# Performance work log

Hardware: AMD Instinct MI355X
Metric: run time of the kernel (lower is better)

The kernel has to match this reference:

```python
import jax, jax.numpy as jnp
import numpy as np

B, N, E = 128, 256, 2048
BINS = 16

def _gcn(x, src, dst, W, b):
    # GCNConv with self-loops and symmetric deg^-1/2 normalization (PyG default).
    h = x @ W  # [N, Fout]
    deg = jnp.zeros(x.shape[0], x.dtype).at[dst].add(1.0) + 1.0  # +1 self-loop
    dinv = jax.lax.rsqrt(deg)
    coef = dinv[src] * dinv[dst]  # [E]
    agg = jnp.zeros_like(h).at[dst].add(h[src] * coef[:, None])
    return agg + h / deg[:, None] + b  # self-loop norm = 1/deg

def _gnn(x, ei, W1, b1, W2, b2, W3, b3):
    # x: [B,N,Fin], ei: [B,2,E]. Dropout skipped (eval mode).
    def single(x, ei):
        s, d = ei[0], ei[1]
        h = jax.nn.relu(_gcn(x, s, d, W1, b1))
        h = jax.nn.relu(_gcn(h, s, d, W2, b2))
        return _gcn(h, s, d, W3, b3)
    return jax.vmap(single)(x, ei)

def _att_pool(x, Watt):
    # SimGNN attention pooling; all graphs have exactly N nodes.
    ctx = jnp.tanh((x @ Watt.T).sum(axis=1) / jnp.asarray(N, x.dtype))  # [B,f3]
    scores = jax.nn.sigmoid(jnp.einsum('bnf,bf->bn', x, ctx))  # [B,N]
    return jnp.einsum('bnf,bn->bf', x, scores)  # [B,f3]

def _forward(xq, xc, eq, ec, W1, b1, W2, b2, W3, b3, Watt, ntnW, ntnV, ntnb, fc1W, fc1b, fc2W, fc2b):
    q = _gnn(xq, eq, W1, b1, W2, b2, W3, b3)  # [B,N,f3]
    c = _gnn(xc, ec, W1, b1, W2, b2, W3, b3)
    e1 = _att_pool(q, Watt)
    e2 = _att_pool(c, Watt)
    # NTN: bilinear + linear on concat + bias
    scores = jax.nn.relu(
        jnp.einsum('bi,tij,bj->bt', e1, ntnW, e2)
        + jnp.concatenate([e1, e2], axis=-1) @ ntnV.T
        + ntnb
    )  # [B, tensor_neurons]
    # histogram of all pairwise node-embedding dot products (torch.histc semantics)
    s = jnp.einsum('bnf,bmf->bnm', q, c).ravel()
    lo, hi = s.min(), s.max()
    idx = jnp.clip(jnp.floor((s - lo) / (hi - lo) * BINS).astype(jnp.int32), 0, BINS - 1)
    counts = jnp.zeros(BINS, s.dtype).at[idx].add(1.0)
    h = jax.lax.stop_gradient(counts / counts.sum())
    scores = jnp.concatenate([scores, jnp.broadcast_to(h, (scores.shape[0], BINS))], axis=1)
    scores = jax.nn.relu(scores @ fc1W.T + fc1b)
    p = jax.nn.sigmoid(scores @ fc2W.T + fc2b)  # [B,1]
    return p.squeeze()


def setup_inputs() -> dict:
    key = jax.random.key(0)
    ks = jax.random.split(key, 20)
    Fin, f1, f2, f3, T, BN = 128, 128, 64, 32, 16, 16
    def xav(k, shape):
        fan_in, fan_out = shape[-1], shape[0]
        lim = np.sqrt(6.0 / (fan_in + fan_out))
        return jax.random.uniform(k, shape, jnp.float32, -lim, lim)
    return {
        'xq': jax.random.normal(ks[0], (B, N, Fin), jnp.float32),
        'xc': jax.random.normal(ks[1], (B, N, Fin), jnp.float32),
        'eq': jax.random.randint(ks[2], (B, 2, E), 0, N, jnp.int32),
        'ec': jax.random.randint(ks[3], (B, 2, E), 0, N, jnp.int32),
        'W1': xav(ks[4], (Fin, f1)), 'b1': jnp.zeros((f1,), jnp.float32),
        'W2': xav(ks[5], (f1, f2)), 'b2': jnp.zeros((f2,), jnp.float32),
        'W3': xav(ks[6], (f2, f3)), 'b3': jnp.zeros((f3,), jnp.float32),
        'Watt': xav(ks[7], (f3, f3)),
        'ntnW': xav(ks[8], (T, f3, f3)),
        'ntnV': xav(ks[9], (T, 2 * f3)),
        'ntnb': xav(ks[10], (T, 1)).squeeze(-1),
        'fc1W': xav(ks[11], (BN, T + BINS)), 'fc1b': jnp.zeros((BN,), jnp.float32),
        'fc2W': xav(ks[12], (1, BN)), 'fc2b': jnp.zeros((1,), jnp.float32),
    }


def reference(xq, xc, eq, ec, W1, b1, W2, b2, W3, b3, Watt, ntnW, ntnV, ntnb, fc1W, fc1b, fc2W, fc2b):
    return _forward(xq, xc, eq, ec, W1, b1, W2, b2, W3, b3, Watt, ntnW, ntnV, ntnb, fc1W, fc1b, fc2W, fc2b)
```

## Files before the change

### kernel.cpp

```cpp
#include <hip/hip_runtime.h>
#include <math.h>

#define BB 128
#define NN 256
#define EE 2048
#define BINS 16

__global__ void csr_kernel(const int* __restrict__ eq, const int* __restrict__ ec,
                           int* __restrict__ off, int* __restrict__ srcs,
                           float* __restrict__ wts) {
    int g = blockIdx.x;
    int b = g < BB ? g : g - BB;
    const int* ei = g < BB ? eq : ec;
    int t = threadIdx.x;
    __shared__ int cnt[NN];
    __shared__ int sa[NN], sb[NN];
    __shared__ int cursor[NN];
    __shared__ float dvs[NN];
    cnt[t] = 0;
    __syncthreads();
    const int* src = ei + b * 2 * EE;
    const int* dst = src + EE;
    for (int e = t; e < EE; e += 256) atomicAdd(&cnt[dst[e]], 1);
    __syncthreads();
    dvs[t] = rsqrtf((float)cnt[t] + 1.0f);
    sa[t] = cnt[t];
    __syncthreads();
    int* pin = sa; int* pout = sb;
    for (int d = 1; d < NN; d <<= 1) {
        int v = pin[t];
        if (t >= d) v += pin[t - d];
        pout[t] = v;
        __syncthreads();
        int* tmp = pin; pin = pout; pout = tmp;
    }
    int excl = pin[t] - cnt[t];
    off[g * 257 + t] = excl;
    if (t == 255) off[g * 257 + 256] = EE;
    cursor[t] = excl;
    __syncthreads();
    for (int e = t; e < EE; e += 256) {
        int d = dst[e], s = src[e];
        int pos = atomicAdd(&cursor[d], 1);
        srcs[g * EE + pos] = s;
        wts[g * EE + pos] = dvs[s] * dvs[d];
    }
}

template<int FIN, int FOUT, bool RELU>
__global__ __launch_bounds__(512) void gcn_fused(
        const float* __restrict__ X0, const float* __restrict__ X1,
        const float* __restrict__ W, const float* __restrict__ bias,
        const int* __restrict__ off, const int* __restrict__ srcs,
        const float* __restrict__ wts, float* __restrict__ OUT) {
    int blk = blockIdx.x;
    int g = blk % (2 * BB);
    int cb = (blk / (2 * BB)) * 32;
    int t = threadIdx.x;

    __shared__ float hT[NN * 33];
    __shared__ float xsT[16 * 260];
    __shared__ float wt[16 * 32];
    __shared__ int   eoff[NN + 1];
    __shared__ int   esrc[EE];
    __shared__ float ewt[EE];

    const float* xg = (g < BB) ? (X0 + (size_t)g * NN * FIN)
                               : (X1 + (size_t)(g - BB) * NN * FIN);
    const int* o = off + g * 257;
    const int* sr = srcs + (size_t)g * EE;
    const float* wg = wts + (size_t)g * EE;

    for (int i = t; i < EE; i += 512) { esrc[i] = sr[i]; ewt[i] = wg[i]; }
    for (int i = t; i <= NN; i += 512) eoff[i] = o[i];

    int l = t & 63;
    int wv = t >> 6;

    float acc[4][4];
#pragma unroll
    for (int i = 0; i < 4; i++)
#pragma unroll
        for (int j = 0; j < 4; j++) acc[i][j] = 0.f;

    int sn = t >> 1, qk = (t & 1) * 8;
    const float* xr = xg + sn * FIN + qk;
    float4 v0 = *(const float4*)xr;
    float4 v1 = *(const float4*)(xr + 4);
    float wreg = W[(t >> 5) * FOUT + cb + (t & 31)];

    for (int k0 = 0; k0 < FIN; k0 += 16) {
        xsT[(qk + 0) * 260 + sn] = v0.x;
        xsT[(qk + 1) * 260 + sn] = v0.y;
        xsT[(qk + 2) * 260 + sn] = v0.z;
        xsT[(qk + 3) * 260 + sn] = v0.w;
        xsT[(qk + 4) * 260 + sn] = v1.x;
        xsT[(qk + 5) * 260 + sn] = v1.y;
        xsT[(qk + 6) * 260 + sn] = v1.z;
        xsT[(qk + 7) * 260 + sn] = v1.w;
        wt[t] = wreg;
        __syncthreads();
        if (k0 + 16 < FIN) {
            xr += 16;
            v0 = *(const float4*)xr;
            v1 = *(const float4*)(xr + 4);
            wreg = W[(k0 + 16 + (t >> 5)) * FOUT + cb + (t & 31)];
        }
#pragma unroll
        for (int k = 0; k < 16; k++) {
            float4 xv = *(const float4*)&xsT[k * 260 + 4 * l];
            float4 wvv = *(const float4*)&wt[k * 32 + 4 * wv];
            acc[0][0] += xv.x * wvv.x; acc[0][1] += xv.x * wvv.y;
            acc[0][2] += xv.x * wvv.z; acc[0][3] += xv.x * wvv.w;
            acc[1][0] += xv.y * wvv.x; acc[1][1] += xv.y * wvv.y;
            acc[1][2] += xv.y * wvv.z; acc[1][3] += xv.y * wvv.w;
            acc[2][0] += xv.z * wvv.x; acc[2][1] += xv.z * wvv.y;
            acc[2][2] += xv.z * wvv.z; acc[2][3] += xv.z * wvv.w;
            acc[3][0] += xv.w * wvv.x; acc[3][1] += xv.w * wvv.y;
            acc[3][2] += xv.w * wvv.z; acc[3][3] += xv.w * wvv.w;
        }
        __syncthreads();
    }
#pragma unroll
    for (int i = 0; i < 4; i++)
#pragma unroll
        for (int j = 0; j < 4; j++)
            hT[(4 * l + i) * 33 + 4 * wv + j] = acc[i][j];
    __syncthreads();

    int c = t & 31, ng = t >> 5;
    float bb_ = bias[cb + c];
    float* outp = OUT + (size_t)g * NN * FOUT;
    for (int n = ng; n < NN; n += 16) {
        int j0 = eoff[n], j1 = eoff[n + 1];
        float a = 0.f;
        for (int j = j0; j < j1; j++) a += hT[esrc[j] * 33 + c] * ewt[j];
        float d0 = rsqrtf((float)(j1 - j0) + 1.0f);
        float val = a + hT[n * 33 + c] * d0 * d0 + bb_;
        if (RELU) val = fmaxf(val, 0.f);
        outp[n * FOUT + cb + c] = val;
    }
}

__global__ void attpool_kernel(const float* __restrict__ X, const float* __restrict__ Watt,
                               float* __restrict__ e) {
    int g = blockIdx.x;
    int t = threadIdx.x;
    __shared__ float xs[NN * 33];
    __shared__ float red[256];
    __shared__ float mean_s[32], ctx_s[32], sc[NN];
    const float* x = X + (size_t)g * NN * 32;
    for (int i = t; i < NN * 32; i += 256) { int n = i >> 5, c = i & 31; xs[n * 33 + c] = x[i]; }
    __syncthreads();
    {
        int c = t & 31, p = t >> 5;
        float s = 0.f;
        for (int n = p * 32; n < (p + 1) * 32; n++) s += xs[n * 33 + c];
        red[t] = s;
    }
    __syncthreads();
    if (t < 32) {
        float m = 0.f;
        for (int p = 0; p < 8; p++) m += red[p * 32 + t];
        mean_s[t] = m / (float)NN;
    }
    __syncthreads();
    if (t < 32) {
        float a = 0.f;
        for (int f = 0; f < 32; f++) a += mean_s[f] * Watt[t * 32 + f];
        ctx_s[t] = tanhf(a);
    }
    __syncthreads();
    {
        float a = 0.f;
        for (int f = 0; f < 32; f++) a += xs[t * 33 + f] * ctx_s[f];
        sc[t] = 1.f / (1.f + expf(-a));
    }
    __syncthreads();
    {
        int c = t & 31, p = t >> 5;
        float s = 0.f;
        for (int n = p * 32; n < (p + 1) * 32; n++) s += xs[n * 33 + c] * sc[n];
        red[t] = s;
    }
    __syncthreads();
    if (t < 32) {
        float s = 0.f;
        for (int p = 0; p < 8; p++) s += red[p * 32 + t];
        e[g * 32 + t] = s;
    }
}

__global__ void pairdot_minmax(const float* __restrict__ Q, const float* __restrict__ C,
                               float* __restrict__ bmin, float* __restrict__ bmax) {
    int blk = blockIdx.x;
    int b = blk / 16;
    int tn = (blk % 16) >> 2, tm = blk & 3;
    __shared__ float qs[64 * 33], cs[64 * 33];
    int t = threadIdx.x;
    const float* q = Q + ((size_t)b * NN + tn * 64) * 32;
    const float* c = C + ((size_t)b * NN + tm * 64) * 32;
    for (int i = t; i < 64 * 32; i += 256) {
        int n = i >> 5, f = i & 31;
        qs[n * 33 + f] = q[i];
        cs[n * 33 + f] = c[i];
    }
    __syncthreads();
    int m = t & 63, n0 = t >> 6;
    float acc[16];
#pragma unroll
    for (int i = 0; i < 16; i++) acc[i] = 0.f;
    for (int f = 0; f < 32; f++) {
        float cv = cs[m * 33 + f];
#pragma unroll
        for (int i = 0; i < 16; i++) acc[i] += qs[(n0 + 4 * i) * 33 + f] * cv;
    }
    float lmin = acc[0], lmax = acc[0];
#pragma unroll
    for (int i = 1; i < 16; i++) {
        lmin = fminf(lmin, acc[i]);
        lmax = fmaxf(lmax, acc[i]);
    }
    __shared__ float rmin[256], rmax[256];
    rmin[t] = lmin; rmax[t] = lmax;
    __syncthreads();
    for (int s = 128; s > 0; s >>= 1) {
        if (t < s) { rmin[t] = fminf(rmin[t], rmin[t + s]); rmax[t] = fmaxf(rmax[t], rmax[t + s]); }
        __syncthreads();
    }
    if (t == 0) { bmin[blk] = rmin[0]; bmax[blk] = rmax[0]; }
}

__global__ void minmax_kernel(const float* __restrict__ bmin, const float* __restrict__ bmax,
                              float* __restrict__ lohi, float* __restrict__ counts) {
    __shared__ float rmin[256], rmax[256];
    int t = threadIdx.x;
    float lmin = 1e30f, lmax = -1e30f;
    for (int i = t; i < 2048; i += 256) { lmin = fminf(lmin, bmin[i]); lmax = fmaxf(lmax, bmax[i]); }
    rmin[t] = lmin; rmax[t] = lmax;
    __syncthreads();
    for (int s = 128; s > 0; s >>= 1) {
        if (t < s) { rmin[t] = fminf(rmin[t], rmin[t + s]); rmax[t] = fmaxf(rmax[t], rmax[t + s]); }
        __syncthreads();
    }
    if (t == 0) { lohi[0] = rmin[0]; lohi[1] = rmax[0]; }
    if (t < BINS) counts[t] = 0.f;
}

__global__ void pairdot_hist(const float* __restrict__ Q, const float* __restrict__ C,
                             const float* __restrict__ lohi, float* __restrict__ counts) {
    int blk = blockIdx.x;
    int b = blk / 16;
    int tn = (blk % 16) >> 2, tm = blk & 3;
    __shared__ float qs[64 * 33], cs[64 * 33];
    int t = threadIdx.x;
    const float* q = Q + ((size_t)b * NN + tn * 64) * 32;
    const float* c = C + ((size_t)b * NN + tm * 64) * 32;
    for (int i = t; i < 64 * 32; i += 256) {
        int n = i >> 5, f = i & 31;
        qs[n * 33 + f] = q[i];
        cs[n * 33 + f] = c[i];
    }
    __syncthreads();
    int m = t & 63, n0 = t >> 6;
    float acc[16];
#pragma unroll
    for (int i = 0; i < 16; i++) acc[i] = 0.f;
    for (int f = 0; f < 32; f++) {
        float cv = cs[m * 33 + f];
#pragma unroll
        for (int i = 0; i < 16; i++) acc[i] += qs[(n0 + 4 * i) * 33 + f] * cv;
    }
    float lo = lohi[0], hi = lohi[1];
    float scale = (float)BINS / (hi - lo);
    int lane = t & 63;
    int cnt = 0;
#pragma unroll
    for (int i = 0; i < 16; i++) {
        int idx = (int)floorf((acc[i] - lo) * scale);
        idx = min(max(idx, 0), BINS - 1);
        unsigned long long b0 = __ballot((idx & 1) != 0);
        unsigned long long b1 = __ballot((idx & 2) != 0);
        unsigned long long b2 = __ballot((idx & 4) != 0);
        unsigned long long b3 = __ballot((idx & 8) != 0);
        unsigned long long msk = ((lane & 1) ? b0 : ~b0);
        msk &= ((lane & 2) ? b1 : ~b1);
        msk &= ((lane & 4) ? b2 : ~b2);
        msk &= ((lane & 8) ? b3 : ~b3);
        cnt += __popcll(msk);
    }
    __shared__ float wbins[4][BINS];
    int wave = t >> 6;
    if (lane < BINS) wbins[wave][lane] = (float)cnt;
    __syncthreads();
    if (t < BINS) {
        atomicAdd(&counts[t], wbins[0][t] + wbins[1][t] + wbins[2][t] + wbins[3][t]);
    }
}

__global__ void final_kernel(const float* __restrict__ e1, const float* __restrict__ e2,
                             const float* __restrict__ ntnW, const float* __restrict__ ntnV,
                             const float* __restrict__ ntnb, const float* __restrict__ counts,
                             const float* __restrict__ fc1W, const float* __restrict__ fc1b,
                             const float* __restrict__ fc2W, const float* __restrict__ fc2b,
                             float* __restrict__ out) {
    int b = blockIdx.x;
    int t = threadIdx.x;
    __shared__ float a1[32], a2[32], red[256], z[32], u[16];
    if (t < 32) a1[t] = e1[b * 32 + t];
    else if (t < 64) a2[t - 32] = e2[b * 32 + t - 32];
    __syncthreads();
    int tt = t >> 4, g = t & 15;
    float p = 0.f;
#pragma unroll
    for (int ii = 0; ii < 2; ii++) {
        int i = g + 16 * ii;
        float d = 0.f;
        const float* wr = ntnW + (tt * 32 + i) * 32;
        for (int j = 0; j < 32; j++) d += wr[j] * a2[j];
        p += a1[i] * d;
    }
    red[t] = p;
    __syncthreads();
    if (t < 16) {
        float s = 0.f;
        for (int g2 = 0; g2 < 16; g2++) s += red[t * 16 + g2];
        float lin = ntnb[t];
        for (int i = 0; i < 32; i++) lin += ntnV[t * 64 + i] * a1[i];
        for (int i = 0; i < 32; i++) lin += ntnV[t * 64 + 32 + i] * a2[i];
        z[t] = fmaxf(s + lin, 0.f);
    } else if (t < 32) {
        float tot = 0.f;
        for (int i = 0; i < BINS; i++) tot += counts[i];
        z[t] = counts[t - 16] / tot;
    }
    __syncthreads();
    if (t < 16) {
        float a = fc1b[t];
        for (int i = 0; i < 32; i++) a += fc1W[t * 32 + i] * z[i];
        u[t] = fmaxf(a, 0.f);
    }
    __syncthreads();
    if (t == 0) {
        float a = fc2b[0];
        for (int i = 0; i < 16; i++) a += fc2W[i] * u[i];
        out[b] = 1.f / (1.f + expf(-a));
    }
}

extern "C" void kernel_launch(void* const* d_in, const int* in_sizes, int n_in,
                              void* d_out, int out_size, void* d_ws, size_t ws_size,
                              hipStream_t stream) {
    const float* xq   = (const float*)d_in[0];
    const float* xc   = (const float*)d_in[1];
    const int*   eq   = (const int*)d_in[2];
    const int*   ec   = (const int*)d_in[3];
    const float* W1   = (const float*)d_in[4];
    const float* b1   = (const float*)d_in[5];
    const float* W2   = (const float*)d_in[6];
    const float* b2   = (const float*)d_in[7];
    const float* W3   = (const float*)d_in[8];
    const float* b3   = (const float*)d_in[9];
    const float* Watt = (const float*)d_in[10];
    const float* ntnW = (const float*)d_in[11];
    const float* ntnV = (const float*)d_in[12];
    const float* ntnb = (const float*)d_in[13];
    const float* fc1W = (const float*)d_in[14];
    const float* fc1b = (const float*)d_in[15];
    const float* fc2W = (const float*)d_in[16];
    const float* fc2b = (const float*)d_in[17];
    float* out = (float*)d_out;
    float* ws  = (float*)d_ws;

    float* O3   = ws;
    float* e12  = O3 + 2097152;
    float* bmin = e12 + 8192;
    float* bmax = bmin + 2048;
    float* lohi = bmax + 2048;
    float* cntw = lohi + 2;
    int*   off  = (int*)(ws + 2109504);
    int*   srcs = off + 65792;
    float* wts  = (float*)(srcs + 524288);
    float* O1   = ws + 3223872;
    float* O2   = O1 + 8388608;

    float* O3Q = O3;
    float* O3C = O3 + (size_t)BB * NN * 32;
    float* e1w = e12;
    float* e2w = e12 + BB * 32;

    csr_kernel<<<2 * BB, 256, 0, stream>>>(eq, ec, off, srcs, wts);

    gcn_fused<128, 128, true><<<4 * 2 * BB, 512, 0, stream>>>(
        xq, xc, W1, b1, off, srcs, wts, O1);
    gcn_fused<128, 64, true><<<2 * 2 * BB, 512, 0, stream>>>(
        O1, O1 + (size_t)BB * NN * 128, W2, b2, off, srcs, wts, O2);
    gcn_fused<64, 32, false><<<1 * 2 * BB, 512, 0, stream>>>(
        O2, O2 + (size_t)BB * NN * 64, W3, b3, off, srcs, wts, O3);

    attpool_kernel<<<2 * BB, 256, 0, stream>>>(O3, Watt, e12);

    pairdot_minmax<<<BB * 16, 256, 0, stream>>>(O3Q, O3C, bmin, bmax);
    minmax_kernel<<<1, 256, 0, stream>>>(bmin, bmax, lohi, cntw);
    pairdot_hist<<<BB * 16, 256, 0, stream>>>(O3Q, O3C, lohi, cntw);

    final_kernel<<<BB, 256, 0, stream>>>(e1w, e2w, ntnW, ntnV, ntnb, cntw,
                                         fc1W, fc1b, fc2W, fc2b, out);
}
```

Measured before the change: 309.9 us.

## Retile GCN and pairwise-dot kernels with larger per-thread register tiles

The fused GCN kernel now runs 256 threads per block instead of 512. Each thread computes a 4x8 output tile, the hT row stride is padded to 36 so rows can be written as float4, and the neighbour-aggregation loop is software-pipelined with a reciprocal replacing rsqrt squared. The pairwise-dot min/max and histogram kernels switch from 64x64 to 128x128 tiles, stage transposed Q/C through shared memory and give each thread an 8x8 register tile, so four times fewer blocks are launched. The aim is more FMA work per shared-memory load and less redundant staging. The cost is higher register pressure and possibly lower occupancy or parallelism.

```diff
diff --git a/kernel.cpp b/kernel.cpp
--- a/kernel.cpp
+++ b/kernel.cpp
@@ -5,6 +5,7 @@
 #define NN 256
 #define EE 2048
 #define BINS 16
+#define HTS 36
 
 __global__ void csr_kernel(const int* __restrict__ eq, const int* __restrict__ ec,
                            int* __restrict__ off, int* __restrict__ srcs,
@@ -48,7 +49,7 @@
 }
 
 template<int FIN, int FOUT, bool RELU>
-__global__ __launch_bounds__(512) void gcn_fused(
+__global__ __launch_bounds__(256, 2) void gcn_fused2(
         const float* __restrict__ X0, const float* __restrict__ X1,
         const float* __restrict__ W, const float* __restrict__ bias,
         const int* __restrict__ off, const int* __restrict__ srcs,
@@ -58,7 +59,7 @@
     int cb = (blk / (2 * BB)) * 32;
     int t = threadIdx.x;
 
-    __shared__ float hT[NN * 33];
+    __shared__ float hT[NN * HTS];
     __shared__ float xsT[16 * 260];
     __shared__ float wt[16 * 32];
     __shared__ int   eoff[NN + 1];
@@ -71,72 +72,83 @@
     const int* sr = srcs + (size_t)g * EE;
     const float* wg = wts + (size_t)g * EE;
 
-    for (int i = t; i < EE; i += 512) { esrc[i] = sr[i]; ewt[i] = wg[i]; }
-    for (int i = t; i <= NN; i += 512) eoff[i] = o[i];
+    for (int i = t; i < EE; i += 256) { esrc[i] = sr[i]; ewt[i] = wg[i]; }
+    for (int i = t; i <= NN; i += 256) eoff[i] = o[i];
 
     int l = t & 63;
     int wv = t >> 6;
 
-    float acc[4][4];
+    float acc[4][8];
 #pragma unroll
     for (int i = 0; i < 4; i++)
 #pragma unroll
-        for (int j = 0; j < 4; j++) acc[i][j] = 0.f;
-
-    int sn = t >> 1, qk = (t & 1) * 8;
-    const float* xr = xg + sn * FIN + qk;
-    float4 v0 = *(const float4*)xr;
-    float4 v1 = *(const float4*)(xr + 4);
-    float wreg = W[(t >> 5) * FOUT + cb + (t & 31)];
+        for (int j = 0; j < 8; j++) acc[i][j] = 0.f;
+
+    const float* xr = xg + t * FIN;
+    float xa[16];
+    *(float4*)&xa[0]  = *(const float4*)(xr);
+    *(float4*)&xa[4]  = *(const float4*)(xr + 4);
+    *(float4*)&xa[8]  = *(const float4*)(xr + 8);
+    *(float4*)&xa[12] = *(const float4*)(xr + 12);
+    int wrow = t >> 4, wcol = (t & 15) * 2;
+    float2 wreg = *(const float2*)&W[wrow * FOUT + cb + wcol];
 
     for (int k0 = 0; k0 < FIN; k0 += 16) {
-        xsT[(qk + 0) * 260 + sn] = v0.x;
-        xsT[(qk + 1) * 260 + sn] = v0.y;
-        xsT[(qk + 2) * 260 + sn] = v0.z;
-        xsT[(qk + 3) * 260 + sn] = v0.w;
-        xsT[(qk + 4) * 260 + sn] = v1.x;
-        xsT[(qk + 5) * 260 + sn] = v1.y;
-        xsT[(qk + 6) * 260 + sn] = v1.z;
-        xsT[(qk + 7) * 260 + sn] = v1.w;
-        wt[t] = wreg;
+#pragma unroll
+        for (int m = 0; m < 16; m++) xsT[m * 260 + t] = xa[m];
+        *(float2*)&wt[wrow * 32 + wcol] = wreg;
         __syncthreads();
         if (k0 + 16 < FIN) {
             xr += 16;
-            v0 = *(const float4*)xr;
-            v1 = *(const float4*)(xr + 4);
-            wreg = W[(k0 + 16 + (t >> 5)) * FOUT + cb + (t & 31)];
+            *(float4*)&xa[0]  = *(const float4*)(xr);
+            *(float4*)&xa[4]  = *(const float4*)(xr + 4);
+            *(float4*)&xa[8]  = *(const float4*)(xr + 8);
+            *(float4*)&xa[12] = *(const float4*)(xr + 12);
+            wreg = *(const float2*)&W[(k0 + 16 + wrow) * FOUT + cb + wcol];
         }
 #pragma unroll
         for (int k = 0; k < 16; k++) {
             float4 xv = *(const float4*)&xsT[k * 260 + 4 * l];
-            float4 wvv = *(const float4*)&wt[k * 32 + 4 * wv];
-            acc[0][0] += xv.x * wvv.x; acc[0][1] += xv.x * wvv.y;
-            acc[0][2] += xv.x * wvv.z; acc[0][3] += xv.x * wvv.w;
-            acc[1][0] += xv.y * wvv.x; acc[1][1] += xv.y * wvv.y;
-            acc[1][2] += xv.y * wvv.z; acc[1][3] += xv.y * wvv.w;
-            acc[2][0] += xv.z * wvv.x; acc[2][1] += xv.z * wvv.y;
-            acc[2][2] += xv.z * wvv.z; acc[2][3] += xv.z * wvv.w;
-            acc[3][0] += xv.w * wvv.x; acc[3][1] += xv.w * wvv.y;
-            acc[3][2] += xv.w * wvv.z; acc[3][3] += xv.w * wvv.w;
+            float4 wa = *(const float4*)&wt[k * 32 + 8 * wv];
+            float4 wb = *(const float4*)&wt[k * 32 + 8 * wv + 4];
+            float xq4[4] = {xv.x, xv.y, xv.z, xv.w};
+            float wc8[8] = {wa.x, wa.y, wa.z, wa.w, wb.x, wb.y, wb.z, wb.w};
+#pragma unroll
+            for (int i = 0; i < 4; i++)
+#pragma unroll
+                for (int j = 0; j < 8; j++) acc[i][j] += xq4[i] * wc8[j];
         }
         __syncthreads();
     }
 #pragma unroll
-    for (int i = 0; i < 4; i++)
-#pragma unroll
-        for (int j = 0; j < 4; j++)
-            hT[(4 * l + i) * 33 + 4 * wv + j] = acc[i][j];
+    for (int i = 0; i < 4; i++) {
+        *(float4*)&hT[(4 * l + i) * HTS + 8 * wv] =
+            make_float4(acc[i][0], acc[i][1], acc[i][2], acc[i][3]);
+        *(float4*)&hT[(4 * l + i) * HTS + 8 * wv + 4] =
+            make_float4(acc[i][4], acc[i][5], acc[i][6], acc[i][7]);
+    }
     __syncthreads();
 
     int c = t & 31, ng = t >> 5;
     float bb_ = bias[cb + c];
     float* outp = OUT + (size_t)g * NN * FOUT;
-    for (int n = ng; n < NN; n += 16) {
+    for (int n = ng; n < NN; n += 8) {
         int j0 = eoff[n], j1 = eoff[n + 1];
         float a = 0.f;
-        for (int j = j0; j < j1; j++) a += hT[esrc[j] * 33 + c] * ewt[j];
-        float d0 = rsqrtf((float)(j1 - j0) + 1.0f);
-        float val = a + hT[n * 33 + c] * d0 * d0 + bb_;
+        int j = j0;
+        if (j < j1) {
+            int s0 = esrc[j];
+            float w0 = ewt[j];
+            for (++j; j < j1; ++j) {
+                int s1 = esrc[j];
+                float w1 = ewt[j];
+                a += hT[s0 * HTS + c] * w0;
+                s0 = s1; w0 = w1;
+            }
+            a += hT[s0 * HTS + c] * w0;
+        }
+        float d0i = 1.0f / ((float)(j1 - j0) + 1.0f);
+        float val = a + hT[n * HTS + c] * d0i + bb_;
         if (RELU) val = fmaxf(val, 0.f);
         outp[n * FOUT + cb + c] = val;
     }
@@ -191,36 +203,65 @@
     }
 }
 
-__global__ void pairdot_minmax(const float* __restrict__ Q, const float* __restrict__ C,
-                               float* __restrict__ bmin, float* __restrict__ bmax) {
-    int blk = blockIdx.x;
-    int b = blk / 16;
-    int tn = (blk % 16) >> 2, tm = blk & 3;
-    __shared__ float qs[64 * 33], cs[64 * 33];
-    int t = threadIdx.x;
-    const float* q = Q + ((size_t)b * NN + tn * 64) * 32;
-    const float* c = C + ((size_t)b * NN + tm * 64) * 32;
-    for (int i = t; i < 64 * 32; i += 256) {
-        int n = i >> 5, f = i & 31;
-        qs[n * 33 + f] = q[i];
-        cs[n * 33 + f] = c[i];
-    }
-    __syncthreads();
-    int m = t & 63, n0 = t >> 6;
-    float acc[16];
-#pragma unroll
-    for (int i = 0; i < 16; i++) acc[i] = 0.f;
-    for (int f = 0; f < 32; f++) {
-        float cv = cs[m * 33 + f];
-#pragma unroll
-        for (int i = 0; i < 16; i++) acc[i] += qs[(n0 + 4 * i) * 33 + f] * cv;
-    }
-    float lmin = acc[0], lmax = acc[0];
-#pragma unroll
-    for (int i = 1; i < 16; i++) {
-        lmin = fminf(lmin, acc[i]);
-        lmax = fmaxf(lmax, acc[i]);
-    }
+#define PD_STAGE_AND_DOT \
+    int blk = blockIdx.x; \
+    int b = blk >> 2; \
+    int tq = (blk >> 1) & 1, tc = blk & 1; \
+    __shared__ float qsT[32 * 132]; \
+    __shared__ float csT[32 * 132]; \
+    int t = threadIdx.x; \
+    { \
+        int n = t >> 1, f0 = (t & 1) * 16; \
+        const float* qp = Q + ((size_t)b * NN + tq * 128 + n) * 32 + f0; \
+        const float* cp = C + ((size_t)b * NN + tc * 128 + n) * 32 + f0; \
+        float qa16[16], ca16[16]; \
+        *(float4*)&qa16[0]  = *(const float4*)(qp); \
+        *(float4*)&qa16[4]  = *(const float4*)(qp + 4); \
+        *(float4*)&qa16[8]  = *(const float4*)(qp + 8); \
+        *(float4*)&qa16[12] = *(const float4*)(qp + 12); \
+        *(float4*)&ca16[0]  = *(const float4*)(cp); \
+        *(float4*)&ca16[4]  = *(const float4*)(cp + 4); \
+        *(float4*)&ca16[8]  = *(const float4*)(cp + 8); \
+        *(float4*)&ca16[12] = *(const float4*)(cp + 12); \
+        _Pragma("unroll") \
+        for (int m = 0; m < 16; m++) { \
+            qsT[(f0 + m) * 132 + n] = qa16[m]; \
+            csT[(f0 + m) * 132 + n] = ca16[m]; \
+        } \
+    } \
+    __syncthreads(); \
+    int rg = (t >> 4) * 4, cg = (t & 15) * 4; \
+    float acc[8][8]; \
+    _Pragma("unroll") \
+    for (int i = 0; i < 8; i++) \
+        _Pragma("unroll") \
+        for (int j = 0; j < 8; j++) acc[i][j] = 0.f; \
+    _Pragma("unroll 2") \
+    for (int f = 0; f < 32; f++) { \
+        float4 qa = *(const float4*)&qsT[f * 132 + rg]; \
+        float4 qb = *(const float4*)&qsT[f * 132 + 64 + rg]; \
+        float4 ca = *(const float4*)&csT[f * 132 + cg]; \
+        float4 cb = *(const float4*)&csT[f * 132 + 64 + cg]; \
+        float qv[8] = {qa.x, qa.y, qa.z, qa.w, qb.x, qb.y, qb.z, qb.w}; \
+        float cv[8] = {ca.x, ca.y, ca.z, ca.w, cb.x, cb.y, cb.z, cb.w}; \
+        _Pragma("unroll") \
+        for (int i = 0; i < 8; i++) \
+            _Pragma("unroll") \
+            for (int j = 0; j < 8; j++) acc[i][j] += qv[i] * cv[j]; \
+    }
+
+__global__ __launch_bounds__(256, 4) void pairdot_minmax(
+        const float* __restrict__ Q, const float* __restrict__ C,
+        float* __restrict__ bmin, float* __restrict__ bmax) {
+    PD_STAGE_AND_DOT
+    float lmin = acc[0][0], lmax = acc[0][0];
+#pragma unroll
+    for (int i = 0; i < 8; i++)
+#pragma unroll
+        for (int j = 0; j < 8; j++) {
+            lmin = fminf(lmin, acc[i][j]);
+            lmax = fmaxf(lmax, acc[i][j]);
+        }
     __shared__ float rmin[256], rmax[256];
     rmin[t] = lmin; rmax[t] = lmax;
     __syncthreads();
@@ -236,7 +277,7 @@
     __shared__ float rmin[256], rmax[256];
     int t = threadIdx.x;
     float lmin = 1e30f, lmax = -1e30f;
-    for (int i = t; i < 2048; i += 256) { lmin = fminf(lmin, bmin[i]); lmax = fmaxf(lmax, bmax[i]); }
+    for (int i = t; i < 512; i += 256) { lmin = fminf(lmin, bmin[i]); lmax = fmaxf(lmax, bmax[i]); }
     rmin[t] = lmin; rmax[t] = lmax;
     __syncthreads();
     for (int s = 128; s > 0; s >>= 1) {
@@ -247,48 +288,30 @@
     if (t < BINS) counts[t] = 0.f;
 }
 
-__global__ void pairdot_hist(const float* __restrict__ Q, const float* __restrict__ C,
-                             const float* __restrict__ lohi, float* __restrict__ counts) {
-    int blk = blockIdx.x;
-    int b = blk / 16;
-    int tn = (blk % 16) >> 2, tm = blk & 3;
-    __shared__ float qs[64 * 33], cs[64 * 33];
-    int t = threadIdx.x;
-    const float* q = Q + ((size_t)b * NN + tn * 64) * 32;
-    const float* c = C + ((size_t)b * NN + tm * 64) * 32;
-    for (int i = t; i < 64 * 32; i += 256) {
-        int n = i >> 5, f = i & 31;
-        qs[n * 33 + f] = q[i];
-        cs[n * 33 + f] = c[i];
-    }
-    __syncthreads();
-    int m = t & 63, n0 = t >> 6;
-    float acc[16];
-#pragma unroll
-    for (int i = 0; i < 16; i++) acc[i] = 0.f;
-    for (int f = 0; f < 32; f++) {
-        float cv = cs[m * 33 + f];
-#pragma unroll
-        for (int i = 0; i < 16; i++) acc[i] += qs[(n0 + 4 * i) * 33 + f] * cv;
-    }
+__global__ __launch_bounds__(256, 4) void pairdot_hist(
+        const float* __restrict__ Q, const float* __restrict__ C,
+        const float* __restrict__ lohi, float* __restrict__ counts) {
+    PD_STAGE_AND_DOT
     float lo = lohi[0], hi = lohi[1];
     float scale = (float)BINS / (hi - lo);
     int lane = t & 63;
     int cnt = 0;
 #pragma unroll
-    for (int i = 0; i < 16; i++) {
-        int idx = (int)floorf((acc[i] - lo) * scale);
-        idx = min(max(idx, 0), BINS - 1);
-        unsigned long long b0 = __ballot((idx & 1) != 0);
-        unsigned long long b1 = __ballot((idx & 2) != 0);
-        unsigned long long b2 = __ballot((idx & 4) != 0);
-        unsigned long long b3 = __ballot((idx & 8) != 0);
-        unsigned long long msk = ((lane & 1) ? b0 : ~b0);
-        msk &= ((lane & 2) ? b1 : ~b1);
-        msk &= ((lane & 4) ? b2 : ~b2);
-        msk &= ((lane & 8) ? b3 : ~b3);
-        cnt += __popcll(msk);
-    }
+    for (int i = 0; i < 8; i++)
+#pragma unroll
+        for (int j = 0; j < 8; j++) {
+            int idx = (int)floorf((acc[i][j] - lo) * scale);
+            idx = min(max(idx, 0), BINS - 1);
+            unsigned long long b0 = __ballot((idx & 1) != 0);
+            unsigned long long b1 = __ballot((idx & 2) != 0);
+            unsigned long long b2 = __ballot((idx & 4) != 0);
+            unsigned long long b3 = __ballot((idx & 8) != 0);
+            unsigned long long msk = ((lane & 1) ? b0 : ~b0);
+            msk &= ((lane & 2) ? b1 : ~b1);
+            msk &= ((lane & 4) ? b2 : ~b2);
+            msk &= ((lane & 8) ? b3 : ~b3);
+            cnt += __popcll(msk);
+        }
     __shared__ float wbins[4][BINS];
     int wave = t >> 6;
     if (lane < BINS) wbins[wave][lane] = (float)cnt;
@@ -391,18 +414,18 @@
 
     csr_kernel<<<2 * BB, 256, 0, stream>>>(eq, ec, off, srcs, wts);
 
-    gcn_fused<128, 128, true><<<4 * 2 * BB, 512, 0, stream>>>(
+    gcn_fused2<128, 128, true><<<4 * 2 * BB, 256, 0, stream>>>(
         xq, xc, W1, b1, off, srcs, wts, O1);
-    gcn_fused<128, 64, true><<<2 * 2 * BB, 512, 0, stream>>>(
+    gcn_fused2<128, 64, true><<<2 * 2 * BB, 256, 0, stream>>>(
         O1, O1 + (size_t)BB * NN * 128, W2, b2, off, srcs, wts, O2);
-    gcn_fused<64, 32, false><<<1 * 2 * BB, 512, 0, stream>>>(
+    gcn_fused2<64, 32, false><<<1 * 2 * BB, 256, 0, stream>>>(
         O2, O2 + (size_t)BB * NN * 64, W3, b3, off, srcs, wts, O3);
 
     attpool_kernel<<<2 * BB, 256, 0, stream>>>(O3, Watt, e12);
 
-    pairdot_minmax<<<BB * 16, 256, 0, stream>>>(O3Q, O3C, bmin, bmax);
+    pairdot_minmax<<<BB * 4, 256, 0, stream>>>(O3Q, O3C, bmin, bmax);
     minmax_kernel<<<1, 256, 0, stream>>>(bmin, bmax, lohi, cntw);
-    pairdot_hist<<<BB * 16, 256, 0, stream>>>(O3Q, O3C, lohi, cntw);
+    pairdot_hist<<<BB * 4, 256, 0, stream>>>(O3Q, O3C, lohi, cntw);
 
     final_kernel<<<BB, 256, 0, stream>>>(e1w, e2w, ntnW, ntnV, ntnb, cntw,
                                          fc1W, fc1b, fc2W, fc2b, out);
```

Result: no change. 309.9 us (+0.0%).
